# Kernel optimization log

Measured on AMD Instinct MI355X. Metric: run time of the kernel, lower is better.

## Reference

```python
import jax, jax.numpy as jnp
import numpy as np

EMBED_DIM = 256
N, S, T = 4, 4096, 4096


def setup_inputs() -> dict:
    key = jax.random.key(0)
    ks = jax.random.split(key, 9)
    D = EMBED_DIM
    scale = 1.0 / np.sqrt(D)
    inp = {
        "query": jax.random.normal(ks[0], (N, S, D), dtype=jnp.float32),
        "key": jax.random.normal(ks[1], (N, T, D), dtype=jnp.float32),
        "value": jax.random.normal(ks[2], (N, T, D), dtype=jnp.float32),
        # Linear params (torch nn.Linear: y = x @ W.T + b)
        "Wq": jax.random.normal(ks[3], (D, D), dtype=jnp.float32) * scale,
        "bq": jax.random.normal(ks[4], (D,), dtype=jnp.float32) * scale,
        "Wk": jax.random.normal(ks[5], (D, D), dtype=jnp.float32) * scale,
        "bk": jax.random.normal(ks[6], (D,), dtype=jnp.float32) * scale,
        "Wv": jax.random.normal(ks[7], (D, D), dtype=jnp.float32) * scale,
        "bv": jax.random.normal(ks[8], (D,), dtype=jnp.float32) * scale,
    }
    return inp


def reference(query, key, value, Wq, bq, Wk, bk, Wv, bv):
    D = query.shape[-1]
    q = jnp.einsum('nsd,ed->nse', query, Wq) + bq   # [N,S,D]
    k = jnp.einsum('ntd,ed->nte', key, Wk) + bk     # [N,T,D]
    v = jnp.einsum('ntd,ed->nte', value, Wv) + bv   # [N,T,D]
    scores = jnp.einsum('nsd,ntd->nst', q, k) / jnp.sqrt(jnp.float32(D))  # [N,S,T]
    attn = jax.nn.softmax(scores, axis=-1)
    # dropout is identity in eval mode
    y = jnp.einsum('nst,ntd->nsd', attn, v)
    return y
```

## Files before the change

### kernel.cpp

```cpp
#include <hip/hip_runtime.h>
#include <hip/hip_bf16.h>

typedef __attribute__((ext_vector_type(4))) float f32x4;
typedef __attribute__((ext_vector_type(8))) short s16x8;
typedef __attribute__((ext_vector_type(4))) short s16x4;

#define DEV __device__ __forceinline__

DEV unsigned short f2bf(float f) {
  union { float f; unsigned u; } v; v.f = f;
  unsigned r = v.u + 0x7FFFu + ((v.u >> 16) & 1u);
  return (unsigned short)(r >> 16);
}

DEV s16x4 cvt4(const f32x4 a) {
  unsigned u0, u1;
  asm("v_cvt_pk_bf16_f32 %0, %1, %2" : "=v"(u0) : "v"(a[0]), "v"(a[1]));
  asm("v_cvt_pk_bf16_f32 %0, %1, %2" : "=v"(u1) : "v"(a[2]), "v"(a[3]));
  union { s16x4 v; unsigned uu[2]; } r;
  r.uu[0] = u0; r.uu[1] = u1;
  return r.v;
}

__global__ __launch_bounds__(256) void proj_kernel(
    const float* __restrict__ Qx, const float* __restrict__ Kx, const float* __restrict__ Vx,
    const float* __restrict__ Wq, const float* __restrict__ bq,
    const float* __restrict__ Wk, const float* __restrict__ bk,
    const float* __restrict__ Wv, const float* __restrict__ bv,
    unsigned short* __restrict__ qb, unsigned short* __restrict__ kb,
    unsigned short* __restrict__ vt)
{
  const int z = blockIdx.z;
  const float* X = (z == 0) ? Qx : (z == 1) ? Kx : Vx;
  const float* W = (z == 0) ? Wq : (z == 1) ? Wk : Wv;
  const float* B = (z == 0) ? bq : (z == 1) ? bk : bv;
  unsigned short* Y = (z == 0) ? qb : (z == 1) ? kb : vt;
  const int out_mode = (z == 2);

  const int row0 = blockIdx.x * 128;
  const int col0 = blockIdx.y * 128;
  const int tid  = threadIdx.x;
  const int lane = tid & 63;
  const int w    = tid >> 6;
  const int wr = w >> 1, wc = w & 1;
  const int l15 = lane & 15, lg = lane >> 4;

  __shared__ unsigned short As[128][40];
  __shared__ unsigned short Bs[128][40];

  f32x4 acc[4][4];
  #pragma unroll
  for (int i = 0; i < 4; ++i)
    #pragma unroll
    for (int j = 0; j < 4; ++j) acc[i][j] = {0.f, 0.f, 0.f, 0.f};

  const int lr = tid >> 3;
  const int lc = (tid & 7) << 2;

  for (int k0 = 0; k0 < 256; k0 += 32) {
    __syncthreads();
    #pragma unroll
    for (int p = 0; p < 4; ++p) {
      const int r = p * 32 + lr;
      f32x4 a = *reinterpret_cast<const f32x4*>(&X[(size_t)(row0 + r) * 256 + k0 + lc]);
      *reinterpret_cast<s16x4*>(&As[r][lc]) = cvt4(a);
      f32x4 b = *reinterpret_cast<const f32x4*>(&W[(size_t)(col0 + r) * 256 + k0 + lc]);
      *reinterpret_cast<s16x4*>(&Bs[r][lc]) = cvt4(b);
    }
    __syncthreads();
    s16x8 af[4], bf[4];
    #pragma unroll
    for (int mi = 0; mi < 4; ++mi)
      af[mi] = *reinterpret_cast<const s16x8*>(&As[wr * 64 + mi * 16 + l15][lg * 8]);
    #pragma unroll
    for (int ni = 0; ni < 4; ++ni)
      bf[ni] = *reinterpret_cast<const s16x8*>(&Bs[wc * 64 + ni * 16 + l15][lg * 8]);
    #pragma unroll
    for (int mi = 0; mi < 4; ++mi)
      #pragma unroll
      for (int ni = 0; ni < 4; ++ni)
        acc[mi][ni] = __builtin_amdgcn_mfma_f32_16x16x32_bf16(af[mi], bf[ni], acc[mi][ni], 0, 0, 0);
  }

  #pragma unroll
  for (int ni = 0; ni < 4; ++ni) {
    const int col = col0 + wc * 64 + ni * 16 + l15;
    const float bv_ = B[col];
    #pragma unroll
    for (int mi = 0; mi < 4; ++mi)
      #pragma unroll
      for (int j = 0; j < 4; ++j) {
        const int row = row0 + wr * 64 + mi * 16 + lg * 4 + j;
        const unsigned short h = f2bf(acc[mi][ni][j] + bv_);
        if (out_mode == 0) {
          Y[(size_t)row * 256 + col] = h;
        } else {
          const int t  = row & 4095;
          const int tp = (t & ~31) | (((t >> 2) & 3) * 8 + ((t >> 4) & 1) * 4 + (t & 3));
          Y[((size_t)((row >> 12) * 256 + col)) * 4096 + tp] = h;
        }
      }
  }
}

__global__ __launch_bounds__(256, 2) void attn_kernel(
    const unsigned short* __restrict__ Qb,
    const unsigned short* __restrict__ Kb,
    const unsigned short* __restrict__ Vt,
    float* __restrict__ pO, float* __restrict__ pML, const int TS)
{
  __shared__ __align__(16) unsigned short smem[32768];

  const int o   = blockIdx.x;
  const int cpx = gridDim.x >> 3;
  const int wg  = (o & 7) * cpx + (o >> 3);
  const int qtile = wg & 127;
  const int ts    = wg >> 7;
  const int n  = qtile >> 5;
  const int q0 = (qtile & 31) * 128;

  const int tid  = threadIdx.x;
  const int lane = tid & 63;
  const int w    = tid >> 6;
  const int l15  = lane & 15;
  const int lg   = lane >> 4;

  const int range = 4096 / TS;
  const int NT    = range >> 5;
  const int tbase = ts * range;

  const unsigned short* kbase = Kb + ((size_t)n * 4096) * 256;
  const unsigned short* vbase = Vt + ((size_t)n * 256) * 4096;

  unsigned kOff[4], vOff[4];
  #pragma unroll
  for (int ld = 0; ld < 4; ++ld) {
    const int gi  = ld * 256 + w * 64 + lane;
    const int key = gi >> 5, slot = gi & 31;
    kOff[ld] = (unsigned)(key * 256 + (slot ^ (key & 7)) * 8);
    const int d = gi >> 2, gv = gi & 3;
    vOff[ld] = (unsigned)(d * 4096 + ((gv ^ ((d >> 1) & 3)) * 8));
  }

  #define STAGE(BUF, T0)                                                              \
    do {                                                                              \
      unsigned short* kd = &smem[(BUF) * 8192];                                       \
      unsigned short* vd = &smem[16384 + (BUF) * 8192];                               \
      _Pragma("unroll")                                                               \
      for (int ld = 0; ld < 4; ++ld)                                                  \
        __builtin_amdgcn_global_load_lds(                                             \
            (const __attribute__((address_space(1))) unsigned int*)                   \
                (kbase + (size_t)(T0) * 256 + kOff[ld]),                              \
            (__attribute__((address_space(3))) unsigned int*)                         \
                &kd[(ld * 256 + w * 64 + lane) * 8], 16, 0, 0);                       \
      _Pragma("unroll")                                                               \
      for (int ld = 0; ld < 4; ++ld)                                                  \
        __builtin_amdgcn_global_load_lds(                                             \
            (const __attribute__((address_space(1))) unsigned int*)                   \
                (vbase + (size_t)(T0) + vOff[ld]),                                    \
            (__attribute__((address_space(3))) unsigned int*)                         \
                &vd[(ld * 256 + w * 64 + lane) * 8], 16, 0, 0);                       \
    } while (0)

  s16x8 aq[2][8];
  #pragma unroll
  for (int qk = 0; qk < 2; ++qk) {
    const size_t qoff = ((size_t)(n * 4096 + q0 + w * 32 + qk * 16 + l15)) * 256 + lg * 8;
    #pragma unroll
    for (int kg = 0; kg < 8; ++kg)
      aq[qk][kg] = *reinterpret_cast<const s16x8*>(&Qb[qoff + kg * 32]);
  }
  __builtin_amdgcn_sched_barrier(0);
  asm volatile("s_waitcnt vmcnt(0)" ::: "memory");
  __builtin_amdgcn_sched_barrier(0);

  f32x4 o_acc[2][16];
  #pragma unroll
  for (int qk = 0; qk < 2; ++qk)
    #pragma unroll
    for (int dt = 0; dt < 16; ++dt) o_acc[qk][dt] = {0.f, 0.f, 0.f, 0.f};
  f32x4 l_acc[2];
  l_acc[0] = {0.f, 0.f, 0.f, 0.f};
  l_acc[1] = {0.f, 0.f, 0.f, 0.f};

  s16x8 ones;
  #pragma unroll
  for (int i = 0; i < 8; ++i) ones[i] = (short)0x3F80;

  const float c  = 0.09016844005f;
  const float b0 = -8.656170245f;

  STAGE(0, tbase);

  for (int i = 0; i < NT; ++i) {
    const int cur = i & 1;

    __builtin_amdgcn_sched_barrier(0);
    asm volatile("s_waitcnt lgkmcnt(0)" ::: "memory");
    __builtin_amdgcn_sched_barrier(0);
    __builtin_amdgcn_s_barrier();
    __builtin_amdgcn_sched_barrier(0);

    if (i + 1 < NT) {
      STAGE(cur ^ 1, tbase + (i + 1) * 32);
      asm volatile("s_waitcnt vmcnt(8)" ::: "memory");
    } else {
      asm volatile("s_waitcnt vmcnt(0)" ::: "memory");
    }
    __builtin_amdgcn_sched_barrier(0);
    __builtin_amdgcn_s_barrier();
    __builtin_amdgcn_sched_barrier(0);

    const unsigned short* Kt = &smem[cur * 8192];
    const unsigned short* Vw = &smem[16384 + cur * 8192];

    f32x4 s[2][2];
    #pragma unroll
    for (int qk = 0; qk < 2; ++qk) { s[qk][0] = {0.f,0.f,0.f,0.f}; s[qk][1] = {0.f,0.f,0.f,0.f}; }
    __builtin_amdgcn_s_setprio(1);
    #pragma unroll
    for (int nt = 0; nt < 2; ++nt) {
      const int key = nt * 16 + l15;
      #pragma unroll
      for (int kg = 0; kg < 8; ++kg) {
        const s16x8 kf = *reinterpret_cast<const s16x8*>(
            &Kt[key * 256 + (((kg * 4 + lg) ^ (l15 & 7)) * 8)]);
        s[0][nt] = __builtin_amdgcn_mfma_f32_16x16x32_bf16(kf, aq[0][kg], s[0][nt], 0, 0, 0);
        s[1][nt] = __builtin_amdgcn_mfma_f32_16x16x32_bf16(kf, aq[1][kg], s[1][nt], 0, 0, 0);
      }
    }
    __builtin_amdgcn_s_setprio(0);

    s16x8 pb[2];
    #pragma unroll
    for (int qk = 0; qk < 2; ++qk) {
      unsigned u[4];
      #pragma unroll
      for (int h = 0; h < 4; ++h) {
        const int nt = h >> 1, j0 = (h & 1) * 2;
        const float p0 = exp2f(fmaf(s[qk][nt][j0],     c, b0));
        const float p1 = exp2f(fmaf(s[qk][nt][j0 + 1], c, b0));
        asm("v_cvt_pk_bf16_f32 %0, %1, %2" : "=v"(u[h]) : "v"(p0), "v"(p1));
      }
      union { s16x8 v; unsigned uu[4]; } cvt;
      cvt.uu[0] = u[0]; cvt.uu[1] = u[1]; cvt.uu[2] = u[2]; cvt.uu[3] = u[3];
      pb[qk] = cvt.v;
    }

    __builtin_amdgcn_s_setprio(1);
    l_acc[0] = __builtin_amdgcn_mfma_f32_16x16x32_bf16(ones, pb[0], l_acc[0], 0, 0, 0);
    l_acc[1] = __builtin_amdgcn_mfma_f32_16x16x32_bf16(ones, pb[1], l_acc[1], 0, 0, 0);
    #pragma unroll
    for (int dt = 0; dt < 16; ++dt) {
      const int d = dt * 16 + l15;
      const s16x8 vf = *reinterpret_cast<const s16x8*>(
          &Vw[d * 32 + ((lg ^ ((d >> 1) & 3)) * 8)]);
      o_acc[0][dt] = __builtin_amdgcn_mfma_f32_16x16x32_bf16(vf, pb[0], o_acc[0][dt], 0, 0, 0);
      o_acc[1][dt] = __builtin_amdgcn_mfma_f32_16x16x32_bf16(vf, pb[1], o_acc[1][dt], 0, 0, 0);
    }
    __builtin_amdgcn_s_setprio(0);
  }

  #pragma unroll
  for (int qk = 0; qk < 2; ++qk) {
    const size_t r = (size_t)ts * 16384 + n * 4096 + q0 + w * 32 + qk * 16 + l15;
    if (lg == 0) pML[r] = l_acc[qk][0];
    #pragma unroll
    for (int dt = 0; dt < 16; ++dt)
      *reinterpret_cast<f32x4*>(&pO[r * 256 + dt * 16 + lg * 4]) = o_acc[qk][dt];
  }
  #undef STAGE
}

__global__ __launch_bounds__(256) void merge_kernel(
    const float* __restrict__ pO, const float* __restrict__ pML,
    float* __restrict__ out, const int TS)
{
  const int idx = blockIdx.x * 256 + threadIdx.x;
  const int row = idx >> 6;
  const int dp  = (idx & 63) << 2;

  f32x4 num = {0.f, 0.f, 0.f, 0.f};
  float den = 0.f;
  for (int t = 0; t < TS; ++t) {
    den += pML[(size_t)t * 16384 + row];
    const f32x4 o = *reinterpret_cast<const f32x4*>(&pO[((size_t)t * 16384 + row) * 256 + dp]);
    num[0] += o[0]; num[1] += o[1]; num[2] += o[2]; num[3] += o[3];
  }
  const float inv = 1.0f / den;
  f32x4 y = { num[0] * inv, num[1] * inv, num[2] * inv, num[3] * inv };
  *reinterpret_cast<f32x4*>(&out[(size_t)row * 256 + dp]) = y;
}

extern "C" void kernel_launch(void* const* d_in, const int* in_sizes, int n_in,
                              void* d_out, int out_size, void* d_ws, size_t ws_size,
                              hipStream_t stream) {
  const float* query = (const float*)d_in[0];
  const float* key   = (const float*)d_in[1];
  const float* value = (const float*)d_in[2];
  const float* Wq    = (const float*)d_in[3];
  const float* bq    = (const float*)d_in[4];
  const float* Wk    = (const float*)d_in[5];
  const float* bk    = (const float*)d_in[6];
  const float* Wv    = (const float*)d_in[7];
  const float* bv    = (const float*)d_in[8];
  float* out = (float*)d_out;

  unsigned short* qb = (unsigned short*)d_ws;
  unsigned short* kb = qb + (size_t)16384 * 256;
  unsigned short* vt = kb + (size_t)16384 * 256;
  const size_t base    = (size_t)3 * 16384 * 256 * 2;
  const size_t poBytes = (size_t)16384 * 256 * 4;
  const size_t mlBytes = (size_t)16384 * 4;
  const int TS = (ws_size >= base + 4 * (poBytes + mlBytes)) ? 4 : 2;
  float* pO  = (float*)((char*)d_ws + base);
  float* pML = (float*)((char*)d_ws + base + (size_t)TS * poBytes);
  (void)in_sizes; (void)n_in; (void)out_size;

  proj_kernel<<<dim3(128, 2, 3), 256, 0, stream>>>(query, key, value,
                                                   Wq, bq, Wk, bk, Wv, bv,
                                                   qb, kb, vt);
  attn_kernel<<<dim3(128 * TS), 256, 0, stream>>>(qb, kb, vt, pO, pML, TS);
  merge_kernel<<<dim3(4096), 256, 0, stream>>>(pO, pML, out, TS);
}
```

Baseline: 120.9 us.

## Double-buffer projection GEMM LDS tiles with register prefetch of next k-slice

The projection kernel now loads the next 32-wide k-slice of X and W into registers while the current slice is converted to bf16, stored into one of two LDS buffers, and consumed by MFMAs. This hides global load latency behind compute and drops one barrier per iteration, using an explicit lgkmcnt wait plus s_barrier. Launch bounds now request two blocks per CU. The cost is doubled LDS use and extra prefetch registers. The projection is only a small part of total runtime next to attention.

```diff
diff --git a/kernel.cpp b/kernel.cpp
--- a/kernel.cpp
+++ b/kernel.cpp
@@ -22,7 +22,7 @@
   return r.v;
 }
 
-__global__ __launch_bounds__(256) void proj_kernel(
+__global__ __launch_bounds__(256, 2) void proj_kernel(
     const float* __restrict__ Qx, const float* __restrict__ Kx, const float* __restrict__ Vx,
     const float* __restrict__ Wq, const float* __restrict__ bq,
     const float* __restrict__ Wk, const float* __restrict__ bk,
@@ -45,8 +45,8 @@
   const int wr = w >> 1, wc = w & 1;
   const int l15 = lane & 15, lg = lane >> 4;
 
-  __shared__ unsigned short As[128][40];
-  __shared__ unsigned short Bs[128][40];
+  __shared__ unsigned short As[2][128][40];
+  __shared__ unsigned short Bs[2][128][40];
 
   f32x4 acc[4][4];
   #pragma unroll
@@ -57,24 +57,44 @@
   const int lr = tid >> 3;
   const int lc = (tid & 7) << 2;
 
-  for (int k0 = 0; k0 < 256; k0 += 32) {
-    __syncthreads();
+  f32x4 ra[4], rb[4];
+  #pragma unroll
+  for (int p = 0; p < 4; ++p) {
+    const int r = p * 32 + lr;
+    ra[p] = *reinterpret_cast<const f32x4*>(&X[(size_t)(row0 + r) * 256 + lc]);
+    rb[p] = *reinterpret_cast<const f32x4*>(&W[(size_t)(col0 + r) * 256 + lc]);
+  }
+
+  for (int ki = 0; ki < 8; ++ki) {
+    const int buf = ki & 1;
     #pragma unroll
     for (int p = 0; p < 4; ++p) {
       const int r = p * 32 + lr;
-      f32x4 a = *reinterpret_cast<const f32x4*>(&X[(size_t)(row0 + r) * 256 + k0 + lc]);
-      *reinterpret_cast<s16x4*>(&As[r][lc]) = cvt4(a);
-      f32x4 b = *reinterpret_cast<const f32x4*>(&W[(size_t)(col0 + r) * 256 + k0 + lc]);
-      *reinterpret_cast<s16x4*>(&Bs[r][lc]) = cvt4(b);
-    }
-    __syncthreads();
+      *reinterpret_cast<s16x4*>(&As[buf][r][lc]) = cvt4(ra[p]);
+      *reinterpret_cast<s16x4*>(&Bs[buf][r][lc]) = cvt4(rb[p]);
+    }
+    if (ki < 7) {
+      const int k0 = (ki + 1) * 32;
+      #pragma unroll
+      for (int p = 0; p < 4; ++p) {
+        const int r = p * 32 + lr;
+        ra[p] = *reinterpret_cast<const f32x4*>(&X[(size_t)(row0 + r) * 256 + k0 + lc]);
+        rb[p] = *reinterpret_cast<const f32x4*>(&W[(size_t)(col0 + r) * 256 + k0 + lc]);
+      }
+    }
+    __builtin_amdgcn_sched_barrier(0);
+    asm volatile("s_waitcnt lgkmcnt(0)" ::: "memory");
+    __builtin_amdgcn_sched_barrier(0);
+    __builtin_amdgcn_s_barrier();
+    __builtin_amdgcn_sched_barrier(0);
+
     s16x8 af[4], bf[4];
     #pragma unroll
     for (int mi = 0; mi < 4; ++mi)
-      af[mi] = *reinterpret_cast<const s16x8*>(&As[wr * 64 + mi * 16 + l15][lg * 8]);
+      af[mi] = *reinterpret_cast<const s16x8*>(&As[buf][wr * 64 + mi * 16 + l15][lg * 8]);
     #pragma unroll
     for (int ni = 0; ni < 4; ++ni)
-      bf[ni] = *reinterpret_cast<const s16x8*>(&Bs[wc * 64 + ni * 16 + l15][lg * 8]);
+      bf[ni] = *reinterpret_cast<const s16x8*>(&Bs[buf][wc * 64 + ni * 16 + l15][lg * 8]);
     #pragma unroll
     for (int mi = 0; mi < 4; ++mi)
       #pragma unroll
```

After: 126.9 us. 4.9% more time.

## Single-buffer V tile, store bf16 partials, and allow eight-way key split

Applied to the files above, without the earlier changes.

Cuts the attention kernel's LDS use by keeping only one V buffer: V for the current tile is now issued at the start of each iteration while K for the next tile is prefetched into a double buffer. Partial outputs are written as bf16 instead of fp32, which halves partial-output traffic, and the merge kernel converts them back. With the smaller partials, the launcher can pick a split of eight over the key range when the workspace is large enough. V loads are less overlapped, and bf16 partials lose some precision before the merge.

```diff
diff --git a/kernel.cpp b/kernel.cpp
--- a/kernel.cpp
+++ b/kernel.cpp
@@ -20,6 +20,12 @@
   union { s16x4 v; unsigned uu[2]; } r;
   r.uu[0] = u0; r.uu[1] = u1;
   return r.v;
+}
+
+DEV float bf2f(unsigned short h) {
+  union { unsigned u; float f; } v;
+  v.u = ((unsigned)h) << 16;
+  return v.f;
 }
 
 __global__ __launch_bounds__(256) void proj_kernel(
@@ -107,9 +113,9 @@
     const unsigned short* __restrict__ Qb,
     const unsigned short* __restrict__ Kb,
     const unsigned short* __restrict__ Vt,
-    float* __restrict__ pO, float* __restrict__ pML, const int TS)
+    unsigned short* __restrict__ pO, float* __restrict__ pML, const int TS)
 {
-  __shared__ __align__(16) unsigned short smem[32768];
+  __shared__ __align__(16) unsigned short smem[24576];
 
   const int o   = blockIdx.x;
   const int cpx = gridDim.x >> 3;
@@ -142,10 +148,9 @@
     vOff[ld] = (unsigned)(d * 4096 + ((gv ^ ((d >> 1) & 3)) * 8));
   }
 
-  #define STAGE(BUF, T0)                                                              \
+  #define STAGE_K(BUF, T0)                                                            \
     do {                                                                              \
       unsigned short* kd = &smem[(BUF) * 8192];                                       \
-      unsigned short* vd = &smem[16384 + (BUF) * 8192];                               \
       _Pragma("unroll")                                                               \
       for (int ld = 0; ld < 4; ++ld)                                                  \
         __builtin_amdgcn_global_load_lds(                                             \
@@ -153,6 +158,11 @@
                 (kbase + (size_t)(T0) * 256 + kOff[ld]),                              \
             (__attribute__((address_space(3))) unsigned int*)                         \
                 &kd[(ld * 256 + w * 64 + lane) * 8], 16, 0, 0);                       \
+    } while (0)
+
+  #define STAGE_V(T0)                                                                 \
+    do {                                                                              \
+      unsigned short* vd = &smem[16384];                                              \
       _Pragma("unroll")                                                               \
       for (int ld = 0; ld < 4; ++ld)                                                  \
         __builtin_amdgcn_global_load_lds(                                             \
@@ -190,20 +200,19 @@
   const float c  = 0.09016844005f;
   const float b0 = -8.656170245f;
 
-  STAGE(0, tbase);
+  STAGE_K(0, tbase);
 
   for (int i = 0; i < NT; ++i) {
-    const int cur = i & 1;
-
     __builtin_amdgcn_sched_barrier(0);
     asm volatile("s_waitcnt lgkmcnt(0)" ::: "memory");
     __builtin_amdgcn_sched_barrier(0);
     __builtin_amdgcn_s_barrier();
     __builtin_amdgcn_sched_barrier(0);
 
+    STAGE_V(tbase + i * 32);
     if (i + 1 < NT) {
-      STAGE(cur ^ 1, tbase + (i + 1) * 32);
-      asm volatile("s_waitcnt vmcnt(8)" ::: "memory");
+      STAGE_K((i + 1) & 1, tbase + (i + 1) * 32);
+      asm volatile("s_waitcnt vmcnt(4)" ::: "memory");
     } else {
       asm volatile("s_waitcnt vmcnt(0)" ::: "memory");
     }
@@ -211,8 +220,8 @@
     __builtin_amdgcn_s_barrier();
     __builtin_amdgcn_sched_barrier(0);
 
-    const unsigned short* Kt = &smem[cur * 8192];
-    const unsigned short* Vw = &smem[16384 + cur * 8192];
+    const unsigned short* Kt = &smem[(i & 1) * 8192];
+    const unsigned short* Vw = &smem[16384];
 
     f32x4 s[2][2];
     #pragma unroll
@@ -267,13 +276,14 @@
     if (lg == 0) pML[r] = l_acc[qk][0];
     #pragma unroll
     for (int dt = 0; dt < 16; ++dt)
-      *reinterpret_cast<f32x4*>(&pO[r * 256 + dt * 16 + lg * 4]) = o_acc[qk][dt];
-  }
-  #undef STAGE
+      *reinterpret_cast<s16x4*>(&pO[r * 256 + dt * 16 + lg * 4]) = cvt4(o_acc[qk][dt]);
+  }
+  #undef STAGE_K
+  #undef STAGE_V
 }
 
 __global__ __launch_bounds__(256) void merge_kernel(
-    const float* __restrict__ pO, const float* __restrict__ pML,
+    const unsigned short* __restrict__ pO, const float* __restrict__ pML,
     float* __restrict__ out, const int TS)
 {
   const int idx = blockIdx.x * 256 + threadIdx.x;
@@ -284,8 +294,11 @@
   float den = 0.f;
   for (int t = 0; t < TS; ++t) {
     den += pML[(size_t)t * 16384 + row];
-    const f32x4 o = *reinterpret_cast<const f32x4*>(&pO[((size_t)t * 16384 + row) * 256 + dp]);
-    num[0] += o[0]; num[1] += o[1]; num[2] += o[2]; num[3] += o[3];
+    const s16x4 o = *reinterpret_cast<const s16x4*>(&pO[((size_t)t * 16384 + row) * 256 + dp]);
+    num[0] += bf2f((unsigned short)o[0]);
+    num[1] += bf2f((unsigned short)o[1]);
+    num[2] += bf2f((unsigned short)o[2]);
+    num[3] += bf2f((unsigned short)o[3]);
   }
   const float inv = 1.0f / den;
   f32x4 y = { num[0] * inv, num[1] * inv, num[2] * inv, num[3] * inv };
@@ -310,10 +323,11 @@
   unsigned short* kb = qb + (size_t)16384 * 256;
   unsigned short* vt = kb + (size_t)16384 * 256;
   const size_t base    = (size_t)3 * 16384 * 256 * 2;
-  const size_t poBytes = (size_t)16384 * 256 * 4;
+  const size_t poBytes = (size_t)16384 * 256 * 2;
   const size_t mlBytes = (size_t)16384 * 4;
-  const int TS = (ws_size >= base + 4 * (poBytes + mlBytes)) ? 4 : 2;
-  float* pO  = (float*)((char*)d_ws + base);
+  const int TS = (ws_size >= base + 8 * (poBytes + mlBytes)) ? 8
+               : (ws_size >= base + 4 * (poBytes + mlBytes)) ? 4 : 2;
+  unsigned short* pO = (unsigned short*)((char*)d_ws + base);
   float* pML = (float*)((char*)d_ws + base + (size_t)TS * poBytes);
   (void)in_sizes; (void)n_in; (void)out_size;
 
```

After: 134.0 us. 1.11x slower.
